# Performance work log

Hardware: AMD Instinct MI355X
Metric: run time of the kernel (lower is better)

Reference implementation:

```python
import jax, jax.numpy as jnp
import numpy as np

SCALES = (32.0, 64.0, 128.0, 256.0)
RATIOS = (0.5, 1.0, 2.0)
STRIDE = 16
KEEP = 2000          # pre-NMS top-k
TOPK = 300           # post-NMS top-k
MIN_SIZE = 16.0
SCORE_THRESH = 0.05
NMS_THRESH = 0.7


def static_anchors():
    a = []
    for s in SCALES:
        for r in RATIOS:
            w = s * r ** 0.5
            h = s / r ** 0.5
            a.append((-w / 2, -h / 2, w / 2, h / 2))
    return jnp.asarray(a, jnp.float32)  # [12,4]


def generate_anchors(h, w):
    base = static_anchors()
    sx = jnp.arange(w, dtype=jnp.float32) * STRIDE + STRIDE / 2
    sy = jnp.arange(h, dtype=jnp.float32) * STRIDE + STRIDE / 2
    yy, xx = jnp.meshgrid(sy, sx, indexing='ij')
    xs, ys = xx.reshape(-1), yy.reshape(-1)
    shifts = jnp.stack((xs, ys, xs, ys), axis=1)            # [HW,4]
    return (base[None, :, :] + shifts[:, None, :]).reshape(-1, 4)  # [HW*12,4]


def apply_deltas(anchors, d):
    # bbox reg weights are all 1.0
    aw = anchors[..., 2] - anchors[..., 0]
    ah = anchors[..., 3] - anchors[..., 1]
    ax = anchors[..., 0] + aw * 0.5
    ay = anchors[..., 1] + ah * 0.5
    x = ax + d[..., 0] * aw
    y = ay + d[..., 1] * ah
    w = aw * jnp.exp(d[..., 2])
    h = ah * jnp.exp(d[..., 3])
    return jnp.stack((x - w * 0.5, y - h * 0.5, x + w * 0.5, y + h * 0.5), axis=-1)


def conv2d(x, w, b, pad):
    y = jax.lax.conv_general_dilated(x, w, (1, 1), [(pad, pad), (pad, pad)],
                                     dimension_numbers=('NCHW', 'OIHW', 'NCHW'))
    return y + b[None, :, None, None]


def nms_fixed(boxes, scores, valid):
    # boxes already sorted by descending score; greedy NMS with fixed shapes.
    area = (boxes[:, 2] - boxes[:, 0]) * (boxes[:, 3] - boxes[:, 1])
    lt = jnp.maximum(boxes[:, None, :2], boxes[None, :, :2])
    rb = jnp.minimum(boxes[:, None, 2:], boxes[None, :, 2:])
    wh = jnp.clip(rb - lt, 0.0)
    inter = wh[..., 0] * wh[..., 1]
    iou = inter / jnp.maximum(area[:, None] + area[None, :] - inter, 1e-6)
    n = boxes.shape[0]

    def body(i, state):
        keep, supp = state
        k = jnp.logical_and(~supp[i], True)
        keep = keep.at[i].set(k)
        supp = jnp.logical_or(supp, jnp.logical_and(k, iou[i] > NMS_THRESH))
        return keep, supp

    keep, _ = jax.lax.fori_loop(0, n, body, (jnp.zeros(n, bool), ~valid))
    masked = jnp.where(keep, scores, -jnp.inf)
    top_s, top_i = jax.lax.top_k(masked, TOPK)
    ok = top_s > -jnp.inf
    out_boxes = jnp.where(ok[:, None], boxes[top_i], 0.0)
    out_scores = jnp.where(ok, top_s, 0.0)
    return out_boxes, out_scores


def rpn_forward(fx, w1, b1, w2, b2, w3, b3, img_h, img_w):
    _, _, H, W = fx.shape
    x = jax.nn.relu(conv2d(fx, w1, b1, 1))        # [1,512,H,W]
    ox = conv2d(x, w2, b2, 0)                     # [1,12,H,W]
    ax = conv2d(x, w3, b3, 0)                     # [1,48,H,W]
    anchors = generate_anchors(H, W)              # [A,4]
    ox = jnp.transpose(ox, (0, 2, 3, 1)).reshape(-1)                     # [A]
    ax = jnp.transpose(ax.reshape(1, 12, 4, H, W), (0, 3, 4, 1, 2)).reshape(-1, 4)  # [A,4]
    px = apply_deltas(anchors, ax)                # [A,4]
    s = jax.nn.sigmoid(ox)
    top_s, idx = jax.lax.top_k(s, KEEP)           # pre-NMS filter
    b = px[idx]
    x1 = jnp.clip(b[:, 0], 0.0, img_w)
    x2 = jnp.clip(b[:, 2], 0.0, img_w)
    y1 = jnp.clip(b[:, 1], 0.0, img_h)
    y2 = jnp.clip(b[:, 3], 0.0, img_h)
    boxes = jnp.stack((x1, y1, x2, y2), axis=1)
    valid = ((x2 - x1) >= MIN_SIZE) & ((y2 - y1) >= MIN_SIZE) & (top_s >= SCORE_THRESH)
    out_boxes, out_scores = nms_fixed(boxes, top_s, valid)
    return jnp.concatenate((out_boxes, out_scores[:, None]), axis=1)  # [TOPK,5]


def setup_inputs() -> dict:
    key = jax.random.key(0)
    ks = jax.random.split(key, 4)
    fx = jax.random.normal(ks[0], (1, 1024, 64, 64), jnp.float32)
    w1 = jax.random.normal(ks[1], (512, 1024, 3, 3), jnp.float32) * 0.01
    w2 = jax.random.normal(ks[2], (12, 512, 1, 1), jnp.float32) * 0.01
    w3 = jax.random.normal(ks[3], (48, 512, 1, 1), jnp.float32) * 0.01
    return {"fx": fx, "w1": w1, "b1": jnp.zeros((512,), jnp.float32),
            "w2": w2, "b2": jnp.zeros((12,), jnp.float32),
            "w3": w3, "b3": jnp.zeros((48,), jnp.float32),
            "img_h": 1024, "img_w": 1024}


def reference(fx, w1, b1, w2, b2, w3, b3, img_h, img_w):
    return rpn_forward(fx, w1, b1, w2, b2, w3, b3, float(img_h), float(img_w))
```

## Files before the change

kernel.cpp:

```cpp
#include <hip/hip_runtime.h>
#include <math.h>

typedef unsigned int u32;
typedef unsigned long long u64;
typedef unsigned short u16;

typedef float f32x16 __attribute__((ext_vector_type(16)));
typedef short bf16x8 __attribute__((ext_vector_type(8)));

#define A_TOTAL 49152
#define NKEEP 2000
#define NTOPK 300
#define SORTN 4096

#define OFF_PACC   0u
#define OFF_POX    8388608u
#define OFF_BOXES  16777216u
#define OFF_SCORES 17563648u
#define OFF_HIST   17760256u
#define OFF_KEYS   18022400u
#define OFF_CAND5  18055168u
#define OFF_MASK   18096128u
#define OFF_MISC   18620416u
#define OFF_PREW   18624512u
#define WS_NEED    46936064ull

__global__ __launch_bounds__(256) void k_init(u32* __restrict__ hist, u64* __restrict__ keys,
                                              u32* __restrict__ misc, float* __restrict__ out) {
    int t = blockIdx.x * 256 + threadIdx.x;
    if (t < 65536) hist[t] = 0u;
    if (t < SORTN) keys[t] = 0ull;
    if (t < NTOPK * 5) out[t] = 0.f;
    if (t == 0) misc[0] = 0u;
}

__device__ __forceinline__ u16 f2bf(float v) {
    u32 u = __float_as_uint(v);
    return (u16)((u + 0x7FFFu + ((u >> 16) & 1u)) >> 16);
}
__device__ __forceinline__ float bf2f(u16 h) { return __uint_as_float(((u32)h) << 16); }
__device__ __forceinline__ void split3(float v, u16& h, u16& m, u16& l) {
    h = f2bf(v);
    float r1 = v - bf2f(h);
    m = f2bf(r1);
    float r2 = r1 - bf2f(m);
    l = f2bf(r2);
}
__device__ __forceinline__ bf16x8 ldsfrag(const u16* p) {
    const u64* q = (const u64*)p;
    union { u64 w[2]; bf16x8 v; } x;
    x.w[0] = q[0];
    x.w[1] = q[1];
    return x.v;
}
__device__ __forceinline__ void gll16(const void* g, void* l) {
    __builtin_amdgcn_global_load_lds((const __attribute__((address_space(1))) void*)g,
                                     (__attribute__((address_space(3))) void*)l, 16, 0, 0);
}
__device__ __forceinline__ void gll4(const void* g, void* l) {
    __builtin_amdgcn_global_load_lds((const __attribute__((address_space(1))) void*)g,
                                     (__attribute__((address_space(3))) void*)l, 4, 0, 0);
}

__global__ __launch_bounds__(256) void k_splitw(const float* __restrict__ w1, uint4* __restrict__ preW) {
    int u = blockIdx.x * 256 + threadIdx.x;
    int co = u & 63;
    int r1 = u >> 6;
    int g = r1 & 1;
    int r2 = r1 >> 1;
    int tap = r2 % 9;
    int r3 = r2 / 9;
    int c = r3 & 31;
    int r4 = r3 >> 5;
    int yb = r4 & 7;
    int kh = r4 >> 3;
    int ci0 = kh * 512 + c * 16 + g * 8;
    const float* wp = w1 + (size_t)(yb * 64 + co) * 9216 + (size_t)ci0 * 9 + tap;
    union { u16 q[8]; uint4 v; } H, M, L;
#pragma unroll
    for (int i = 0; i < 8; i++) {
        u16 h, m, l;
        split3(wp[i * 9], h, m, l);
        H.q[i] = h; M.q[i] = m; L.q[i] = l;
    }
    size_t base = (size_t)(((kh * 8 + yb) * 32 + c) * 3) * 1152 + (size_t)((tap * 2 + g) * 64 + co);
    preW[base] = H.v;
    preW[base + 1152] = M.v;
    preW[base + 2304] = L.v;
}

__global__ __launch_bounds__(512) void k_conv1m(const float* __restrict__ fx, const uint4* __restrict__ preW,
                                                float* __restrict__ pacc) {
    __shared__ __align__(16) u16 sA[3 * 9216];
    __shared__ __align__(16) u16 sB[3 * 3600];
    u32* const sB32 = (u32*)sB;
    const int tid = threadIdx.x;
    const int lane = tid & 63;
    const int wid = tid >> 6;
    const int cgw = wid >> 2;
    const int pgw = wid & 3;
    const int n = lane & 31;
    const int g = lane >> 5;
    const int bid = blockIdx.x;
    const int yb = bid & 7;
    const int rest = bid >> 3;
    const int bpx = rest & 31;
    const int kh = rest >> 5;
    const int y0 = (bpx >> 2) * 8, x0 = (bpx & 3) * 16;
    const int ci_base = kh * 512;

    int fgp[3], flp[3];
    bool wrp[3], ldp[3];
#pragma unroll
    for (int j = 0; j < 3; j++) {
        int p = tid + j * 512;
        bool wr = p < 1440;
        int a = p / 180, rem = p - a * 180;
        int hy = rem / 18, hx = rem - hy * 18;
        int gy = y0 + hy - 1, gx = x0 + hx - 1;
        bool ok = wr && gy >= 0 && gy < 64 && gx >= 0 && gx < 64;
        wrp[j] = wr;
        ldp[j] = ok;
        fgp[j] = ok ? ((2 * a) * 4096 + gy * 64 + gx) : 0;
        flp[j] = wr ? (rem * 10 + a) : 0;
    }

    f32x16 acc;
    double accD[16];
#pragma unroll
    for (int i = 0; i < 16; i++) { acc[i] = 0.f; accD[i] = 0.0; }

    float pA0[3], pA1[3], pB0[3], pB1[3];
    {
        const float* f0 = fx + (size_t)ci_base * 4096;
        const float* f1 = fx + (size_t)(ci_base + 16) * 4096;
#pragma unroll
        for (int j = 0; j < 3; j++) {
            pA0[j] = ldp[j] ? f0[fgp[j]] : 0.f;
            pA1[j] = ldp[j] ? f0[fgp[j] + 4096] : 0.f;
            pB0[j] = ldp[j] ? f1[fgp[j]] : 0.f;
            pB1[j] = ldp[j] ? f1[fgp[j] + 4096] : 0.f;
        }
    }
    const char* wbase = (const char*)preW + (size_t)((kh * 8 + yb) * 32) * 3 * 18432;
    char* const sAc = (char*)sA;

#pragma unroll 1
    for (int c = 0; c < 32; c++) {
        __syncthreads();
        const char* wsrc = wbase + (size_t)c * 3 * 18432;
#pragma unroll
        for (int s = 0; s < 3; s++) {
            gll16(wsrc + s * 18432 + tid * 16,         sAc + s * 18432 + wid * 1024);
            gll16(wsrc + s * 18432 + 8192 + tid * 16,  sAc + s * 18432 + 8192 + wid * 1024);
            gll4 (wsrc + s * 18432 + 16384 + tid * 4,  sAc + s * 18432 + 16384 + wid * 256);
        }
#pragma unroll
        for (int j = 0; j < 3; j++) {
            if (wrp[j]) {
                u16 h0, m0, l0, h1, m1, l1;
                split3(pA0[j], h0, m0, l0);
                split3(pA1[j], h1, m1, l1);
                sB32[flp[j]] = (u32)h0 | ((u32)h1 << 16);
                sB32[1800 + flp[j]] = (u32)m0 | ((u32)m1 << 16);
                sB32[3600 + flp[j]] = (u32)l0 | ((u32)l1 << 16);
            }
        }
        __syncthreads();
#pragma unroll
        for (int j = 0; j < 3; j++) { pA0[j] = pB0[j]; pA1[j] = pB1[j]; }
        if (c < 30) {
            const float* fp = fx + (size_t)(ci_base + (c + 2) * 16) * 4096;
#pragma unroll
            for (int j = 0; j < 3; j++) {
                pB0[j] = ldp[j] ? fp[fgp[j]] : 0.f;
                pB1[j] = ldp[j] ? fp[fgp[j] + 4096] : 0.f;
            }
        }

#pragma unroll 1
        for (int dy = 0; dy < 3; dy++) {
#pragma unroll
            for (int dx = 0; dx < 3; dx++) {
                const int tap = dy * 3 + dx;
                const int aoff = ((tap * 2 + g) * 64 + cgw * 32 + n) * 8;
                bf16x8 ah = ldsfrag(&sA[aoff]);
                bf16x8 am = ldsfrag(&sA[9216 + aoff]);
                bf16x8 al = ldsfrag(&sA[18432 + aoff]);
                const int loc = (pgw * 2 + (n >> 4) + dy) * 18 + (n & 15) + dx;
                const int boff = loc * 20 + g * 8;
                bf16x8 bh = ldsfrag(&sB[boff]);
                bf16x8 bm = ldsfrag(&sB[3600 + boff]);
                bf16x8 bl = ldsfrag(&sB[7200 + boff]);
                acc = __builtin_amdgcn_mfma_f32_32x32x16_bf16(ah, bh, acc, 0, 0, 0);
                acc = __builtin_amdgcn_mfma_f32_32x32x16_bf16(ah, bm, acc, 0, 0, 0);
                acc = __builtin_amdgcn_mfma_f32_32x32x16_bf16(am, bh, acc, 0, 0, 0);
                acc = __builtin_amdgcn_mfma_f32_32x32x16_bf16(ah, bl, acc, 0, 0, 0);
                acc = __builtin_amdgcn_mfma_f32_32x32x16_bf16(am, bm, acc, 0, 0, 0);
                acc = __builtin_amdgcn_mfma_f32_32x32x16_bf16(al, bh, acc, 0, 0, 0);
            }
#pragma unroll
            for (int i = 0; i < 16; i++) { accD[i] += (double)acc[i]; acc[i] = 0.f; }
        }
    }

    {
        int p = pgw * 32 + n;
        int py = p >> 4, pxx = p & 15;
        int gp = (y0 + py) * 64 + x0 + pxx;
        const int row_hi = 4 * g;
#pragma unroll
        for (int rg = 0; rg < 16; rg++) {
            int co = yb * 64 + cgw * 32 + (rg & 3) + 8 * (rg >> 2) + row_hi;
            pacc[(size_t)kh * 2097152 + (size_t)co * 4096 + gp] = (float)accD[rg];
        }
    }
}

__global__ __launch_bounds__(512) void k_conv1m_fb(const float* __restrict__ fx, const float* __restrict__ w1,
                                                   float* __restrict__ pacc) {
    __shared__ u16 sA[3 * 9472];
    __shared__ u16 sB[3 * 3600];
    u32* const sA32 = (u32*)sA;
    const int tid = threadIdx.x;
    const int lane = tid & 63;
    const int wid = tid >> 6;
    const int cgw = wid >> 2;
    const int pgw = wid & 3;
    const int n = lane & 31;
    const int g = lane >> 5;
    const int bid = blockIdx.x;
    const int yb = bid & 7;
    const int rest = bid >> 3;
    const int bpx = rest & 31;
    const int kh = rest >> 5;
    const int y0 = (bpx >> 2) * 8, x0 = (bpx & 3) * 16;
    const int co0 = yb * 64;
    const int ci_base = kh * 512;

    int wgp[9], wlp[9];
#pragma unroll
    for (int j = 0; j < 9; j++) {
        int p = tid + j * 512;
        int co = p / 72, q = p - co * 72;
        int a = q & 7, b = q >> 3;
        wgp[j] = co * 9216 + (2 * a) * 9 + b;
        wlp[j] = co * 74 + b * 8 + a;
    }
    int fg0[6], fl[6];
#pragma unroll
    for (int j = 0; j < 6; j++) {
        int idx = tid + j * 512;
        bool wr = idx < 2880;
        int ci = idx / 180, rem = idx - ci * 180;
        int hy = rem / 18, hx = rem - hy * 18;
        int gy = y0 + hy - 1, gx = x0 + hx - 1;
        bool ok = wr && gy >= 0 && gy < 64 && gx >= 0 && gx < 64;
        fg0[j] = ok ? (ci * 4096 + gy * 64 + gx) : -1;
        fl[j] = wr ? (rem * 20 + ci) : -1;
    }

    f32x16 acc;
    double accD[16];
#pragma unroll
    for (int i = 0; i < 16; i++) { acc[i] = 0.f; accD[i] = 0.0; }

    float pw[18], pfA[6], pfB[6];
    {
        const float* wp = w1 + (size_t)co0 * 9216 + (size_t)ci_base * 9;
#pragma unroll
        for (int j = 0; j < 9; j++) { pw[2 * j] = wp[wgp[j]]; pw[2 * j + 1] = wp[wgp[j] + 9]; }
        const float* f0 = fx + (size_t)ci_base * 4096;
        const float* f1 = fx + (size_t)(ci_base + 16) * 4096;
#pragma unroll
        for (int j = 0; j < 6; j++) {
            pfA[j] = (fg0[j] >= 0) ? f0[fg0[j]] : 0.f;
            pfB[j] = (fg0[j] >= 0) ? f1[fg0[j]] : 0.f;
        }
    }

#pragma unroll 1
    for (int c = 0; c < 32; c++) {
        __syncthreads();
#pragma unroll
        for (int j = 0; j < 9; j++) {
            u16 h0, m0, l0, h1, m1, l1;
            split3(pw[2 * j], h0, m0, l0);
            split3(pw[2 * j + 1], h1, m1, l1);
            sA32[wlp[j]] = (u32)h0 | ((u32)h1 << 16);
            sA32[4736 + wlp[j]] = (u32)m0 | ((u32)m1 << 16);
            sA32[9472 + wlp[j]] = (u32)l0 | ((u32)l1 << 16);
        }
#pragma unroll
        for (int j = 0; j < 6; j++) {
            if (fl[j] >= 0) {
                u16 h, m, l;
                split3(pfA[j], h, m, l);
                sB[fl[j]] = h; sB[3600 + fl[j]] = m; sB[7200 + fl[j]] = l;
            }
        }
        __syncthreads();
        if (c < 31) {
            const float* wp = w1 + (size_t)co0 * 9216 + (size_t)(ci_base + (c + 1) * 16) * 9;
#pragma unroll
            for (int j = 0; j < 9; j++) { pw[2 * j] = wp[wgp[j]]; pw[2 * j + 1] = wp[wgp[j] + 9]; }
        }
#pragma unroll
        for (int j = 0; j < 6; j++) pfA[j] = pfB[j];
        if (c < 30) {
            const float* fp = fx + (size_t)(ci_base + (c + 2) * 16) * 4096;
#pragma unroll
            for (int j = 0; j < 6; j++) pfB[j] = (fg0[j] >= 0) ? fp[fg0[j]] : 0.f;
        }

#pragma unroll 1
        for (int dy = 0; dy < 3; dy++) {
#pragma unroll
            for (int dx = 0; dx < 3; dx++) {
                const int tap = dy * 3 + dx;
                const int aoff = (cgw * 32 + n) * 148 + tap * 16 + g * 8;
                bf16x8 ah = ldsfrag(&sA[aoff]);
                bf16x8 am = ldsfrag(&sA[9472 + aoff]);
                bf16x8 al = ldsfrag(&sA[18944 + aoff]);
                const int loc = (pgw * 2 + (n >> 4) + dy) * 18 + (n & 15) + dx;
                const int boff = loc * 20 + g * 8;
                bf16x8 bh = ldsfrag(&sB[boff]);
                bf16x8 bm = ldsfrag(&sB[3600 + boff]);
                bf16x8 bl = ldsfrag(&sB[7200 + boff]);
                acc = __builtin_amdgcn_mfma_f32_32x32x16_bf16(ah, bh, acc, 0, 0, 0);
                acc = __builtin_amdgcn_mfma_f32_32x32x16_bf16(ah, bm, acc, 0, 0, 0);
                acc = __builtin_amdgcn_mfma_f32_32x32x16_bf16(am, bh, acc, 0, 0, 0);
                acc = __builtin_amdgcn_mfma_f32_32x32x16_bf16(ah, bl, acc, 0, 0, 0);
                acc = __builtin_amdgcn_mfma_f32_32x32x16_bf16(am, bm, acc, 0, 0, 0);
                acc = __builtin_amdgcn_mfma_f32_32x32x16_bf16(al, bh, acc, 0, 0, 0);
            }
#pragma unroll
            for (int i = 0; i < 16; i++) { accD[i] += (double)acc[i]; acc[i] = 0.f; }
        }
    }

    {
        int p = pgw * 32 + n;
        int py = p >> 4, pxx = p & 15;
        int gp = (y0 + py) * 64 + x0 + pxx;
        const int row_hi = 4 * g;
#pragma unroll
        for (int rg = 0; rg < 16; rg++) {
            int co = co0 + cgw * 32 + (rg & 3) + 8 * (rg >> 2) + row_hi;
            pacc[(size_t)kh * 2097152 + (size_t)co * 4096 + gp] = (float)accD[rg];
        }
    }
}

__global__ __launch_bounds__(256) void k_comb(float* __restrict__ x, const float* __restrict__ p1,
                                              const float* __restrict__ b1) {
    int i = blockIdx.x * 256 + threadIdx.x;
    double v = (double)x[i] + (double)p1[i] + (double)b1[i >> 12];
    x[i] = fmaxf((float)v, 0.f);
}

__global__ __launch_bounds__(256) void k_conv23(const float* __restrict__ x,
                                                const float* __restrict__ w2, const float* __restrict__ w3,
                                                double* __restrict__ pox) {
    __shared__ float xs[32 * 64];
    __shared__ float wsh[60 * 128];
    const int tid = threadIdx.x;
    const int px0 = blockIdx.x * 64;
    const int cib = blockIdx.y * 128;
    const int px = tid & 63;
    const int og = tid >> 6;

#pragma unroll
    for (int k = 0; k < 30; k++) {
        int e = tid + k * 256;
        int o = e >> 7, ci = e & 127;
        float wv = (o < 12) ? w2[o * 512 + cib + ci] : w3[(size_t)(o - 12) * 512 + cib + ci];
        wsh[o * 128 + ci] = wv;
    }

    double acc[15];
#pragma unroll
    for (int j = 0; j < 15; j++) acc[j] = 0.0;

#pragma unroll 1
    for (int ch = 0; ch < 4; ch++) {
        __syncthreads();
#pragma unroll
        for (int k = 0; k < 8; k++) {
            int e = tid + k * 256;
            int ci = e >> 6, p = e & 63;
            xs[ci * 64 + p] = x[(size_t)(cib + ch * 32 + ci) * 4096 + px0 + p];
        }
        __syncthreads();
#pragma unroll 1
        for (int ci = 0; ci < 32; ci++) {
            double xd = (double)xs[ci * 64 + px];
            const float* wrow = &wsh[ch * 32 + ci];
#pragma unroll
            for (int j = 0; j < 15; j++)
                acc[j] = fma(xd, (double)wrow[(og * 15 + j) * 128], acc[j]);
        }
    }
#pragma unroll
    for (int j = 0; j < 15; j++) {
        int o = og * 15 + j;
        pox[((size_t)o * 4 + blockIdx.y) * 4096 + px0 + px] = acc[j];
    }
}

__global__ __launch_bounds__(256) void k_boxes(const double* __restrict__ pox,
                                               const float* __restrict__ b2, const float* __restrict__ b3,
                                               const int* __restrict__ imh, const int* __restrict__ imw,
                                               float* __restrict__ boxes, float* __restrict__ scores,
                                               u32* __restrict__ hist) {
    int idx = blockIdx.x * 256 + threadIdx.x;
    if (idx >= A_TOTAL) return;
    int px = idx / 12, a = idx - px * 12;

    double t = 0.0;
#pragma unroll
    for (int q = 0; q < 4; q++) t += pox[((size_t)a * 4 + q) * 4096 + px];
    float o = (float)(t + (double)b2[a]);
    float s = (float)(1.0 / (1.0 + exp(-(double)o)));
    scores[idx] = s;
    atomicAdd(&hist[__float_as_uint(s) >> 16], 1u);

    float d[4];
#pragma unroll
    for (int c = 0; c < 4; c++) {
        int oo = 12 + a * 4 + c;
        double u = 0.0;
#pragma unroll
        for (int q = 0; q < 4; q++) u += pox[((size_t)oo * 4 + q) * 4096 + px];
        d[c] = (float)(u + (double)b3[a * 4 + c]);
    }

    int py = px >> 6, pxx = px & 63;
    double cx = pxx * 16.0 + 8.0, cy = py * 16.0 + 8.0;
    int si = a / 3, ri = a - si * 3;
    double scale = (double)(32 << si);
    double ratio = 0.5 * (double)(1 << ri);
    double sq = sqrt(ratio);
    double aw = scale * sq, ah = scale / sq;
    double xc = cx + (double)d[0] * aw;
    double yc = cy + (double)d[1] * ah;
    double wv = aw * exp((double)d[2]);
    double hv = ah * exp((double)d[3]);
    float W = (float)imw[0], H = (float)imh[0];
    float x1 = fminf(fmaxf((float)(xc - wv * 0.5), 0.f), W);
    float x2 = fminf(fmaxf((float)(xc + wv * 0.5), 0.f), W);
    float y1 = fminf(fmaxf((float)(yc - hv * 0.5), 0.f), H);
    float y2 = fminf(fmaxf((float)(yc + hv * 0.5), 0.f), H);
    boxes[(size_t)idx * 4 + 0] = x1;
    boxes[(size_t)idx * 4 + 1] = y1;
    boxes[(size_t)idx * 4 + 2] = x2;
    boxes[(size_t)idx * 4 + 3] = y2;
}

__global__ __launch_bounds__(256) void k_scanhist(const u32* __restrict__ hist, u32* __restrict__ misc) {
    __shared__ u32 csum[256];
    __shared__ u32 cb[256];
    __shared__ int s_cidx;
    __shared__ u32 s_cacc;
    int t = threadIdx.x;
    u32 sum = 0;
    const uint4* h4 = (const uint4*)(hist + t * 256);
    for (int j = 0; j < 64; j++) { uint4 v = h4[j]; sum += v.x + v.y + v.z + v.w; }
    csum[t] = sum;
    __syncthreads();
    if (t == 0) {
        u32 acc = 0;
        int c = 255;
        for (; c > 0; c--) {
            if (acc + csum[c] >= NKEEP) break;
            acc += csum[c];
        }
        s_cidx = c;
        s_cacc = acc;
    }
    __syncthreads();
    cb[t] = hist[s_cidx * 256 + t];
    __syncthreads();
    if (t == 0) {
        u32 acc = s_cacc;
        int b = 255;
        for (; b > 0; b--) {
            acc += cb[b];
            if (acc >= NKEEP) break;
        }
        misc[1] = (u32)(s_cidx * 256 + b);
    }
}

__global__ __launch_bounds__(256) void k_compact(const float* __restrict__ scores, u32* __restrict__ misc,
                                                 u64* __restrict__ keys) {
    int idx = blockIdx.x * 256 + threadIdx.x;
    if (idx >= A_TOTAL) return;
    u32 bits = __float_as_uint(scores[idx]);
    if ((bits >> 16) >= misc[1]) {
        u32 slot = atomicAdd(&misc[0], 1u);
        if (slot < SORTN) keys[slot] = ((u64)bits << 32) | (u64)(~(u32)idx);
    }
}

__global__ __launch_bounds__(1024) void k_sort(const u64* __restrict__ keys, const float* __restrict__ boxes,
                                               float* __restrict__ cand5, u64* __restrict__ suppws) {
    __shared__ u64 lk[SORTN];
    int t = threadIdx.x;
#pragma unroll
    for (int r = 0; r < 4; r++) lk[r * 1024 + t] = keys[r * 1024 + t];
    for (int kk = 2; kk <= SORTN; kk <<= 1) {
        for (int jj = kk >> 1; jj > 0; jj >>= 1) {
            __syncthreads();
#pragma unroll
            for (int rep = 0; rep < 4; rep++) {
                int i = rep * 1024 + t;
                int ixj = i ^ jj;
                if (ixj > i) {
                    u64 a = lk[i], b = lk[ixj];
                    bool sw = ((i & kk) == 0) ? (a < b) : (a > b);
                    if (sw) { lk[i] = b; lk[ixj] = a; }
                }
            }
        }
    }
    __syncthreads();
#pragma unroll
    for (int rep = 0; rep < 2; rep++) {
        int i = rep * 1024 + t;
        bool suppb = true;
        float c0 = 0.f, c1 = 0.f, c2 = 0.f, c3 = 0.f, cs = 0.f;
        if (i < NKEEP) {
            u64 key = lk[i];
            u32 idx = ~(u32)(key & 0xFFFFFFFFull);
            cs = __uint_as_float((u32)(key >> 32));
            c0 = boxes[(size_t)idx * 4 + 0];
            c1 = boxes[(size_t)idx * 4 + 1];
            c2 = boxes[(size_t)idx * 4 + 2];
            c3 = boxes[(size_t)idx * 4 + 3];
            bool valid = ((c2 - c0) >= 16.f) && ((c3 - c1) >= 16.f) && (cs >= 0.05f);
            suppb = !valid;
        }
        cand5[i * 5 + 0] = c0;
        cand5[i * 5 + 1] = c1;
        cand5[i * 5 + 2] = c2;
        cand5[i * 5 + 3] = c3;
        cand5[i * 5 + 4] = cs;
        u64 bal = __ballot(suppb ? 1 : 0);
        if ((t & 63) == 0) suppws[i >> 6] = bal;
    }
}

__global__ __launch_bounds__(64) void k_mask(const float* __restrict__ cand5, u64* __restrict__ mask) {
    __shared__ float cb[64][5];
    int t = threadIdx.x;
    int bi = blockIdx.y, bj = blockIdx.x;
    int j = bj * 64 + t;
    {
        float b0 = cand5[j * 5 + 0], b1v = cand5[j * 5 + 1], b2v = cand5[j * 5 + 2], b3v = cand5[j * 5 + 3];
        cb[t][0] = b0; cb[t][1] = b1v; cb[t][2] = b2v; cb[t][3] = b3v;
        cb[t][4] = (b2v - b0) * (b3v - b1v);
    }
    __syncthreads();
    int i = bi * 64 + t;
    float r0 = cand5[i * 5 + 0], r1 = cand5[i * 5 + 1], r2 = cand5[i * 5 + 2], r3 = cand5[i * 5 + 3];
    float ra = (r2 - r0) * (r3 - r1);
    u64 bits = 0ull;
#pragma unroll 4
    for (int c = 0; c < 64; c++) {
        float lx = fmaxf(r0, cb[c][0]);
        float ly = fmaxf(r1, cb[c][1]);
        float rx = fminf(r2, cb[c][2]);
        float ry = fminf(r3, cb[c][3]);
        float w = fmaxf(rx - lx, 0.f);
        float h = fmaxf(ry - ly, 0.f);
        float inter = w * h;
        float iou = inter / fmaxf(ra + cb[c][4] - inter, 1e-6f);
        if (iou > 0.7f) bits |= (1ull << c);
    }
    mask[(size_t)i * 32 + bj] = bits;
}

__global__ __launch_bounds__(64) void k_scan(const u64* __restrict__ mask, const float* __restrict__ cand5,
                                             const u64* __restrict__ suppws, float* __restrict__ out) {
    int lane = threadIdx.x;
    u64 supp = (lane < 32) ? suppws[lane] : 0ull;
    u64 bufA[8], bufB[8];
    float dA[8], dB[8];
#pragma unroll
    for (int k = 0; k < 8; k++) {
        bufA[k] = (lane < 32) ? mask[(size_t)k * 32 + lane] : 0ull;
        dA[k] = (lane < 5) ? cand5[k * 5 + lane] : 0.f;
    }
    int kcount = 0;
    for (int gq = 0; gq < 256; gq++) {
        int base = gq * 8;
        if (gq < 255) {
            int nb = base + 8;
#pragma unroll
            for (int k = 0; k < 8; k++) {
                bufB[k] = (lane < 32) ? mask[(size_t)(nb + k) * 32 + lane] : 0ull;
                dB[k] = (lane < 5) ? cand5[(nb + k) * 5 + lane] : 0.f;
            }
        }
        int w = gq >> 3;
        u64 cur = __shfl(supp, w);
#pragma unroll
        for (int k = 0; k < 8; k++) {
            int i = base + k;
            if (i < NKEEP && !((cur >> (i & 63)) & 1ull)) {
                if (kcount < NTOPK) {
                    if (lane < 5) out[kcount * 5 + lane] = dA[k];
                    kcount++;
                }
                supp |= bufA[k];
                cur |= __shfl(bufA[k], w);
            }
        }
        if (kcount >= NTOPK) return;
#pragma unroll
        for (int k = 0; k < 8; k++) { bufA[k] = bufB[k]; dA[k] = dB[k]; }
    }
}

extern "C" void kernel_launch(void* const* d_in, const int* in_sizes, int n_in,
                              void* d_out, int out_size, void* d_ws, size_t ws_size,
                              hipStream_t stream) {
    (void)in_sizes; (void)n_in; (void)out_size;
    const float* fx = (const float*)d_in[0];
    const float* w1 = (const float*)d_in[1];
    const float* b1 = (const float*)d_in[2];
    const float* w2 = (const float*)d_in[3];
    const float* b2 = (const float*)d_in[4];
    const float* w3 = (const float*)d_in[5];
    const float* b3 = (const float*)d_in[6];
    const int* imh = (const int*)d_in[7];
    const int* imw = (const int*)d_in[8];

    char* ws = (char*)d_ws;
    float*  pacc   = (float*)(ws + OFF_PACC);
    double* pox    = (double*)(ws + OFF_POX);
    float*  boxes  = (float*)(ws + OFF_BOXES);
    float*  scores = (float*)(ws + OFF_SCORES);
    u32*    hist   = (u32*)(ws + OFF_HIST);
    u64*    keys   = (u64*)(ws + OFF_KEYS);
    float*  cand5  = (float*)(ws + OFF_CAND5);
    u64*    mask   = (u64*)(ws + OFF_MASK);
    u32*    misc   = (u32*)(ws + OFF_MISC);
    u64*    suppws = (u64*)(ws + OFF_MISC + 64);
    uint4*  preW   = (uint4*)(ws + OFF_PREW);
    float*  out    = (float*)d_out;

    k_init<<<256, 256, 0, stream>>>(hist, keys, misc, out);
    if (ws_size >= WS_NEED) {
        k_splitw<<<2304, 256, 0, stream>>>(w1, preW);
        k_conv1m<<<512, 512, 0, stream>>>(fx, preW, pacc);
    } else {
        k_conv1m_fb<<<512, 512, 0, stream>>>(fx, w1, pacc);
    }
    k_comb<<<8192, 256, 0, stream>>>(pacc, pacc + 2097152, b1);
    k_conv23<<<dim3(64, 4), 256, 0, stream>>>(pacc, w2, w3, pox);
    k_boxes<<<192, 256, 0, stream>>>(pox, b2, b3, imh, imw, boxes, scores, hist);
    k_scanhist<<<1, 256, 0, stream>>>(hist, misc);
    k_compact<<<192, 256, 0, stream>>>(scores, misc, keys);
    k_sort<<<1, 1024, 0, stream>>>(keys, boxes, cand5, suppws);
    k_mask<<<dim3(32, 32), 64, 0, stream>>>(cand5, mask);
    k_scan<<<1, 64, 0, stream>>>(mask, cand5, suppws, out);
}
```

Before: 481.4 us.

## Fuse bias-ReLU combine into 1x1 heads, decode boxes lazily in sort

Removes the separate k_comb pass by summing the two conv1 partials, adding bias and applying ReLU while loading tiles in the 1x1 head kernel. The head kernel now runs the full 512-channel reduction per block and writes float logits directly, which drops the split-K double partials and the k_boxes reduction. Box decoding moves into the sort kernel and runs only for the 2000 kept candidates. k_splitw is also restructured to stage weights through shared memory so the global writes are coalesced. The trade-off is that the head kernel launches only 64 blocks, so it has much less parallelism than the previous 256-block split.

Result: slower. 538.0 us (+11.7%).

```diff
diff --git a/kernel.cpp b/kernel.cpp
--- a/kernel.cpp
+++ b/kernel.cpp
@@ -14,16 +14,15 @@
 #define SORTN 4096
 
 #define OFF_PACC   0u
-#define OFF_POX    8388608u
-#define OFF_BOXES  16777216u
-#define OFF_SCORES 17563648u
-#define OFF_HIST   17760256u
-#define OFF_KEYS   18022400u
-#define OFF_CAND5  18055168u
-#define OFF_MASK   18096128u
-#define OFF_MISC   18620416u
-#define OFF_PREW   18624512u
-#define WS_NEED    46936064ull
+#define OFF_LOG    16777216u
+#define OFF_SCORES 17760256u
+#define OFF_HIST   17956864u
+#define OFF_KEYS   18219008u
+#define OFF_CAND5  18251776u
+#define OFF_MASK   18292736u
+#define OFF_MISC   18817024u
+#define OFF_PREW   18821120u
+#define WS_NEED    47132672ull
 
 __global__ __launch_bounds__(256) void k_init(u32* __restrict__ hist, u64* __restrict__ keys,
                                               u32* __restrict__ misc, float* __restrict__ out) {
@@ -63,30 +62,31 @@
 }
 
 __global__ __launch_bounds__(256) void k_splitw(const float* __restrict__ w1, uint4* __restrict__ preW) {
-    int u = blockIdx.x * 256 + threadIdx.x;
-    int co = u & 63;
-    int r1 = u >> 6;
-    int g = r1 & 1;
-    int r2 = r1 >> 1;
-    int tap = r2 % 9;
-    int r3 = r2 / 9;
-    int c = r3 & 31;
-    int r4 = r3 >> 5;
-    int yb = r4 & 7;
-    int kh = r4 >> 3;
-    int ci0 = kh * 512 + c * 16 + g * 8;
-    const float* wp = w1 + (size_t)(yb * 64 + co) * 9216 + (size_t)ci0 * 9 + tap;
-    union { u16 q[8]; uint4 v; } H, M, L;
-#pragma unroll
-    for (int i = 0; i < 8; i++) {
+    __shared__ __align__(16) u16 sW[3 * 9216];
+    const int tid = threadIdx.x;
+    const int c = blockIdx.x;
+    const int yb = blockIdx.y;
+    const int kh = blockIdx.z;
+    const float* base = w1 + (size_t)(yb * 64) * 9216 + (size_t)(kh * 512 + c * 16) * 9;
+#pragma unroll
+    for (int j = 0; j < 36; j++) {
+        int e = tid + j * 256;
+        int co = e / 144, r = e - co * 144;
+        int ci = r / 9, tap = r - ci * 9;
+        float v = base[(size_t)co * 9216 + r];
         u16 h, m, l;
-        split3(wp[i * 9], h, m, l);
-        H.q[i] = h; M.q[i] = m; L.q[i] = l;
-    }
-    size_t base = (size_t)(((kh * 8 + yb) * 32 + c) * 3) * 1152 + (size_t)((tap * 2 + g) * 64 + co);
-    preW[base] = H.v;
-    preW[base + 1152] = M.v;
-    preW[base + 2304] = L.v;
+        split3(v, h, m, l);
+        int li = ((tap * 2 + (ci >> 3)) * 64 + co) * 8 + (ci & 7);
+        sW[li] = h; sW[9216 + li] = m; sW[18432 + li] = l;
+    }
+    __syncthreads();
+    const uint4* sw4 = (const uint4*)sW;
+    uint4* dst = preW + (size_t)(((kh * 8 + yb) * 32 + c) * 3) * 1152;
+#pragma unroll
+    for (int j = 0; j < 14; j++) {
+        int e = tid + j * 256;
+        if (e < 3456) dst[e] = sw4[e];
+    }
 }
 
 __global__ __launch_bounds__(512) void k_conv1m(const float* __restrict__ fx, const uint4* __restrict__ preW,
@@ -352,109 +352,69 @@
     }
 }
 
-__global__ __launch_bounds__(256) void k_comb(float* __restrict__ x, const float* __restrict__ p1,
-                                              const float* __restrict__ b1) {
-    int i = blockIdx.x * 256 + threadIdx.x;
-    double v = (double)x[i] + (double)p1[i] + (double)b1[i >> 12];
-    x[i] = fmaxf((float)v, 0.f);
-}
-
-__global__ __launch_bounds__(256) void k_conv23(const float* __restrict__ x,
-                                                const float* __restrict__ w2, const float* __restrict__ w3,
-                                                double* __restrict__ pox) {
+__global__ __launch_bounds__(256) void k_conv23f(const float* __restrict__ pacc,
+                                                 const float* __restrict__ b1,
+                                                 const float* __restrict__ w2, const float* __restrict__ b2,
+                                                 const float* __restrict__ w3, const float* __restrict__ b3,
+                                                 float* __restrict__ logit) {
     __shared__ float xs[32 * 64];
-    __shared__ float wsh[60 * 128];
+    __shared__ float wsh[60 * 32];
     const int tid = threadIdx.x;
     const int px0 = blockIdx.x * 64;
-    const int cib = blockIdx.y * 128;
     const int px = tid & 63;
     const int og = tid >> 6;
 
-#pragma unroll
-    for (int k = 0; k < 30; k++) {
-        int e = tid + k * 256;
-        int o = e >> 7, ci = e & 127;
-        float wv = (o < 12) ? w2[o * 512 + cib + ci] : w3[(size_t)(o - 12) * 512 + cib + ci];
-        wsh[o * 128 + ci] = wv;
-    }
-
     double acc[15];
 #pragma unroll
     for (int j = 0; j < 15; j++) acc[j] = 0.0;
 
 #pragma unroll 1
-    for (int ch = 0; ch < 4; ch++) {
+    for (int ch = 0; ch < 16; ch++) {
         __syncthreads();
+#pragma unroll
+        for (int k = 0; k < 8; k++) {
+            int e = tid + k * 256;
+            if (e < 1920) {
+                int o = e >> 5, ci = e & 31;
+                wsh[o * 32 + ci] = (o < 12) ? w2[o * 512 + ch * 32 + ci]
+                                            : w3[(size_t)(o - 12) * 512 + ch * 32 + ci];
+            }
+        }
 #pragma unroll
         for (int k = 0; k < 8; k++) {
             int e = tid + k * 256;
             int ci = e >> 6, p = e & 63;
-            xs[ci * 64 + p] = x[(size_t)(cib + ch * 32 + ci) * 4096 + px0 + p];
+            size_t gi = (size_t)(ch * 32 + ci) * 4096 + px0 + p;
+            double v = (double)pacc[gi] + (double)pacc[2097152 + gi] + (double)b1[ch * 32 + ci];
+            xs[ci * 64 + p] = fmaxf((float)v, 0.f);
         }
         __syncthreads();
 #pragma unroll 1
         for (int ci = 0; ci < 32; ci++) {
             double xd = (double)xs[ci * 64 + px];
-            const float* wrow = &wsh[ch * 32 + ci];
+            const float* wrow = &wsh[ci];
 #pragma unroll
             for (int j = 0; j < 15; j++)
-                acc[j] = fma(xd, (double)wrow[(og * 15 + j) * 128], acc[j]);
+                acc[j] = fma(xd, (double)wrow[(og * 15 + j) * 32], acc[j]);
         }
     }
 #pragma unroll
     for (int j = 0; j < 15; j++) {
         int o = og * 15 + j;
-        pox[((size_t)o * 4 + blockIdx.y) * 4096 + px0 + px] = acc[j];
-    }
-}
-
-__global__ __launch_bounds__(256) void k_boxes(const double* __restrict__ pox,
-                                               const float* __restrict__ b2, const float* __restrict__ b3,
-                                               const int* __restrict__ imh, const int* __restrict__ imw,
-                                               float* __restrict__ boxes, float* __restrict__ scores,
-                                               u32* __restrict__ hist) {
+        float bias = (o < 12) ? b2[o] : b3[o - 12];
+        logit[(size_t)o * 4096 + px0 + px] = (float)(acc[j] + (double)bias);
+    }
+}
+
+__global__ __launch_bounds__(256) void k_scores(const float* __restrict__ logit,
+                                                float* __restrict__ scores, u32* __restrict__ hist) {
     int idx = blockIdx.x * 256 + threadIdx.x;
     if (idx >= A_TOTAL) return;
     int px = idx / 12, a = idx - px * 12;
-
-    double t = 0.0;
-#pragma unroll
-    for (int q = 0; q < 4; q++) t += pox[((size_t)a * 4 + q) * 4096 + px];
-    float o = (float)(t + (double)b2[a]);
+    float o = logit[(size_t)a * 4096 + px];
     float s = (float)(1.0 / (1.0 + exp(-(double)o)));
     scores[idx] = s;
     atomicAdd(&hist[__float_as_uint(s) >> 16], 1u);
-
-    float d[4];
-#pragma unroll
-    for (int c = 0; c < 4; c++) {
-        int oo = 12 + a * 4 + c;
-        double u = 0.0;
-#pragma unroll
-        for (int q = 0; q < 4; q++) u += pox[((size_t)oo * 4 + q) * 4096 + px];
-        d[c] = (float)(u + (double)b3[a * 4 + c]);
-    }
-
-    int py = px >> 6, pxx = px & 63;
-    double cx = pxx * 16.0 + 8.0, cy = py * 16.0 + 8.0;
-    int si = a / 3, ri = a - si * 3;
-    double scale = (double)(32 << si);
-    double ratio = 0.5 * (double)(1 << ri);
-    double sq = sqrt(ratio);
-    double aw = scale * sq, ah = scale / sq;
-    double xc = cx + (double)d[0] * aw;
-    double yc = cy + (double)d[1] * ah;
-    double wv = aw * exp((double)d[2]);
-    double hv = ah * exp((double)d[3]);
-    float W = (float)imw[0], H = (float)imh[0];
-    float x1 = fminf(fmaxf((float)(xc - wv * 0.5), 0.f), W);
-    float x2 = fminf(fmaxf((float)(xc + wv * 0.5), 0.f), W);
-    float y1 = fminf(fmaxf((float)(yc - hv * 0.5), 0.f), H);
-    float y2 = fminf(fmaxf((float)(yc + hv * 0.5), 0.f), H);
-    boxes[(size_t)idx * 4 + 0] = x1;
-    boxes[(size_t)idx * 4 + 1] = y1;
-    boxes[(size_t)idx * 4 + 2] = x2;
-    boxes[(size_t)idx * 4 + 3] = y2;
 }
 
 __global__ __launch_bounds__(256) void k_scanhist(const u32* __restrict__ hist, u32* __restrict__ misc) {
@@ -503,7 +463,8 @@
     }
 }
 
-__global__ __launch_bounds__(1024) void k_sort(const u64* __restrict__ keys, const float* __restrict__ boxes,
+__global__ __launch_bounds__(1024) void k_sort(const u64* __restrict__ keys, const float* __restrict__ logit,
+                                               const int* __restrict__ imh, const int* __restrict__ imw,
                                                float* __restrict__ cand5, u64* __restrict__ suppws) {
     __shared__ u64 lk[SORTN];
     int t = threadIdx.x;
@@ -525,6 +486,7 @@
         }
     }
     __syncthreads();
+    float W = (float)imw[0], H = (float)imh[0];
 #pragma unroll
     for (int rep = 0; rep < 2; rep++) {
         int i = rep * 1024 + t;
@@ -534,10 +496,26 @@
             u64 key = lk[i];
             u32 idx = ~(u32)(key & 0xFFFFFFFFull);
             cs = __uint_as_float((u32)(key >> 32));
-            c0 = boxes[(size_t)idx * 4 + 0];
-            c1 = boxes[(size_t)idx * 4 + 1];
-            c2 = boxes[(size_t)idx * 4 + 2];
-            c3 = boxes[(size_t)idx * 4 + 3];
+            int px = idx / 12, a = idx - px * 12;
+            float d0 = logit[(size_t)(12 + a * 4 + 0) * 4096 + px];
+            float d1 = logit[(size_t)(12 + a * 4 + 1) * 4096 + px];
+            float d2 = logit[(size_t)(12 + a * 4 + 2) * 4096 + px];
+            float d3 = logit[(size_t)(12 + a * 4 + 3) * 4096 + px];
+            int py = px >> 6, pxx = px & 63;
+            double cx = pxx * 16.0 + 8.0, cy = py * 16.0 + 8.0;
+            int si = a / 3, ri = a - si * 3;
+            double scale = (double)(32 << si);
+            double ratio = 0.5 * (double)(1 << ri);
+            double sq = sqrt(ratio);
+            double aw = scale * sq, ah = scale / sq;
+            double xc = cx + (double)d0 * aw;
+            double yc = cy + (double)d1 * ah;
+            double wv = aw * exp((double)d2);
+            double hv = ah * exp((double)d3);
+            c0 = fminf(fmaxf((float)(xc - wv * 0.5), 0.f), W);
+            c2 = fminf(fmaxf((float)(xc + wv * 0.5), 0.f), W);
+            c1 = fminf(fmaxf((float)(yc - hv * 0.5), 0.f), H);
+            c3 = fminf(fmaxf((float)(yc + hv * 0.5), 0.f), H);
             bool valid = ((c2 - c0) >= 16.f) && ((c3 - c1) >= 16.f) && (cs >= 0.05f);
             suppb = !valid;
         }
@@ -639,8 +617,7 @@
 
     char* ws = (char*)d_ws;
     float*  pacc   = (float*)(ws + OFF_PACC);
-    double* pox    = (double*)(ws + OFF_POX);
-    float*  boxes  = (float*)(ws + OFF_BOXES);
+    float*  logit  = (float*)(ws + OFF_LOG);
     float*  scores = (float*)(ws + OFF_SCORES);
     u32*    hist   = (u32*)(ws + OFF_HIST);
     u64*    keys   = (u64*)(ws + OFF_KEYS);
@@ -653,17 +630,16 @@
 
     k_init<<<256, 256, 0, stream>>>(hist, keys, misc, out);
     if (ws_size >= WS_NEED) {
-        k_splitw<<<2304, 256, 0, stream>>>(w1, preW);
+        k_splitw<<<dim3(32, 8, 2), 256, 0, stream>>>(w1, preW);
         k_conv1m<<<512, 512, 0, stream>>>(fx, preW, pacc);
     } else {
         k_conv1m_fb<<<512, 512, 0, stream>>>(fx, w1, pacc);
     }
-    k_comb<<<8192, 256, 0, stream>>>(pacc, pacc + 2097152, b1);
-    k_conv23<<<dim3(64, 4), 256, 0, stream>>>(pacc, w2, w3, pox);
-    k_boxes<<<192, 256, 0, stream>>>(pox, b2, b3, imh, imw, boxes, scores, hist);
+    k_conv23f<<<64, 256, 0, stream>>>(pacc, b1, w2, b2, w3, b3, logit);
+    k_scores<<<192, 256, 0, stream>>>(logit, scores, hist);
     k_scanhist<<<1, 256, 0, stream>>>(hist, misc);
     k_compact<<<192, 256, 0, stream>>>(scores, misc, keys);
-    k_sort<<<1, 1024, 0, stream>>>(keys, boxes, cand5, suppws);
+    k_sort<<<1, 1024, 0, stream>>>(keys, logit, imh, imw, cand5, suppws);
     k_mask<<<dim3(32, 32), 64, 0, stream>>>(cand5, mask);
     k_scan<<<1, 64, 0, stream>>>(mask, cand5, suppws, out);
 }
```
